# Kernel optimization log

Hardware: AMD Instinct MI355X
Metric: run time of the kernel (lower is better)

The kernel has to match this reference:

```python
import jax, jax.numpy as jnp
import numpy as np

KERNEL = 16
STRIDE = 4


def setup_inputs() -> dict:
    key = jax.random.key(0)
    k1, k2 = jax.random.split(key)
    x = jax.random.normal(k1, (4096, 8192), dtype=jnp.float32)
    # nn.init.uniform_(Or_weight, 0.3, 0.7)
    w = 0.3 + 0.4 * jax.random.uniform(k2, (1, KERNEL), dtype=jnp.float32)
    return {"input": x, "Or_weight": w}


def _eventually(rho):
    # Soft "Eventually" (soft max) over the last axis: softmax-weighted average.
    return jnp.sum(rho * jax.nn.softmax(rho, axis=-1), axis=-1)


def reference(input, Or_weight):
    N, L = input.shape
    out_len = (L - KERNEL) // STRIDE + 1
    starts = jnp.arange(out_len) * STRIDE                      # [out_len]
    idx = starts[:, None] + jnp.arange(KERNEL)[None, :]        # [out_len, k]
    windows = input[:, idx]                                    # [N, out_len, k]
    rho = windows * Or_weight[0][None, None, :]                # [N, out_len, k]
    return _eventually(rho)                                    # [N, out_len]
```

## Files before the change

kernel.cpp:

```cpp
#include <hip/hip_runtime.h>

constexpr int KSZ     = 16;
constexpr int STRIDE  = 4;
constexpr int NROWS   = 4096;
constexpr int LCOLS   = 8192;
constexpr int OUT_LEN = (LCOLS - KSZ) / STRIDE + 1;

__global__ __launch_bounds__(256) void or_conv_kernel(
    const float* __restrict__ x, const float* __restrict__ w,
    float* __restrict__ out)
{
    const int o = blockIdx.x * 256 + threadIdx.x;
    const int n = blockIdx.y;
    if (o >= OUT_LEN) return;

    float wr[KSZ];
#pragma unroll
    for (int k = 0; k < KSZ; ++k) wr[k] = w[k];

    const float4* p = reinterpret_cast<const float4*>(
        x + (size_t)n * LCOLS + (size_t)o * STRIDE);
    float4 a[4];
#pragma unroll
    for (int j = 0; j < 4; ++j) a[j] = p[j];

    const float* win = reinterpret_cast<const float*>(a);

    float se = 0.f, sr = 0.f;
#pragma unroll
    for (int k = 0; k < KSZ; ++k) {
        float rho = win[k] * wr[k];
        float e   = __expf(rho);
        se += e;
        sr  = fmaf(rho, e, sr);
    }

    out[(size_t)n * OUT_LEN + o] = sr / se;
}

extern "C" void kernel_launch(void* const* d_in, const int* in_sizes, int n_in,
                              void* d_out, int out_size, void* d_ws, size_t ws_size,
                              hipStream_t stream)
{
    const float* x = (const float*)d_in[0];
    const float* w = (const float*)d_in[1];
    float* out     = (float*)d_out;

    dim3 block(256);
    dim3 grid((OUT_LEN + 255) / 256, NROWS);
    or_conv_kernel<<<grid, block, 0, stream>>>(x, w, out);
}
```

Before: 30.93 us.

## Stage full input row in swizzled LDS, one block per row

Each block now loads an entire 8192-float row into shared memory once, using an XOR swizzle, then computes all output windows for that row from LDS. Previously each thread read its own overlapping 64-byte window straight from global memory, so every input element was fetched about four times through the cache. The change also swaps the division for a hardware reciprocal and writes outputs with nontemporal stores. It costs 32KB of LDS per block and a barrier, which may limit occupancy.

```diff
diff --git a/kernel.cpp b/kernel.cpp
--- a/kernel.cpp
+++ b/kernel.cpp
@@ -5,37 +5,55 @@
 constexpr int NROWS   = 4096;
 constexpr int LCOLS   = 8192;
 constexpr int OUT_LEN = (LCOLS - KSZ) / STRIDE + 1;
+constexpr int BLOCK   = 512;
+constexpr int NF4     = LCOLS / 4;
 
-__global__ __launch_bounds__(256) void or_conv_kernel(
+__device__ __forceinline__ int swz(int p) { return p ^ ((p >> 3) & 7); }
+
+__global__ __launch_bounds__(BLOCK) void or_conv_kernel(
     const float* __restrict__ x, const float* __restrict__ w,
     float* __restrict__ out)
 {
-    const int o = blockIdx.x * 256 + threadIdx.x;
-    const int n = blockIdx.y;
-    if (o >= OUT_LEN) return;
+    __shared__ float4 smem[NF4];
+
+    const int t = threadIdx.x;
+    const int n = blockIdx.x;
 
     float wr[KSZ];
 #pragma unroll
     for (int k = 0; k < KSZ; ++k) wr[k] = w[k];
 
-    const float4* p = reinterpret_cast<const float4*>(
-        x + (size_t)n * LCOLS + (size_t)o * STRIDE);
-    float4 a[4];
+    const float4* rowp4 = reinterpret_cast<const float4*>(x + (size_t)n * LCOLS);
 #pragma unroll
-    for (int j = 0; j < 4; ++j) a[j] = p[j];
+    for (int j = 0; j < 4; ++j) {
+        const int pos = t + BLOCK * j;
+        smem[swz(pos)] = rowp4[pos];
+    }
+    __syncthreads();
 
-    const float* win = reinterpret_cast<const float*>(a);
-
-    float se = 0.f, sr = 0.f;
+    float* orow = out + (size_t)n * OUT_LEN;
 #pragma unroll
-    for (int k = 0; k < KSZ; ++k) {
-        float rho = win[k] * wr[k];
-        float e   = __expf(rho);
-        se += e;
-        sr  = fmaf(rho, e, sr);
+    for (int i = 0; i < 4; ++i) {
+        const int o = t + BLOCK * i;
+        if (o < OUT_LEN) {
+            float win[KSZ];
+#pragma unroll
+            for (int j = 0; j < 4; ++j) {
+                const float4 v = smem[swz(o + j)];
+                win[4 * j + 0] = v.x; win[4 * j + 1] = v.y;
+                win[4 * j + 2] = v.z; win[4 * j + 3] = v.w;
+            }
+            float se = 0.f, sr = 0.f;
+#pragma unroll
+            for (int k = 0; k < KSZ; ++k) {
+                const float rho = win[k] * wr[k];
+                const float e   = __expf(rho);
+                se += e;
+                sr  = fmaf(rho, e, sr);
+            }
+            __builtin_nontemporal_store(sr * __builtin_amdgcn_rcpf(se), orow + o);
+        }
     }
-
-    out[(size_t)n * OUT_LEN + o] = sr / se;
 }
 
 extern "C" void kernel_launch(void* const* d_in, const int* in_sizes, int n_in,
@@ -46,7 +64,5 @@
     const float* w = (const float*)d_in[1];
     float* out     = (float*)d_out;
 
-    dim3 block(256);
-    dim3 grid((OUT_LEN + 255) / 256, NROWS);
-    or_conv_kernel<<<grid, block, 0, stream>>>(x, w, out);
+    or_conv_kernel<<<dim3(NROWS), dim3(BLOCK), 0, stream>>>(x, w, out);
 }
```

After: 32.36 us. +4.6%, slower.
